# Performance work log

Measured on AMD Instinct MI355X. Metric: run time of the kernel, lower is better.

Reference implementation:

```python
import jax, jax.numpy as jnp
import numpy as np

T, B = 80, 256                 # timesteps (max objs per image), num sequences (images)
OBJ_DIM, EMBED, HID = 4096, 200, 512
NCLS = 151                      # 150 VG classes + background
D = HID + OBJ_DIM + EMBED + 128 # decoder inputs_dim = 4936


def _packed_gather_idx():
    # descending lengths 80..41, mimicking a sorted PackedSequence
    lengths = np.array([T - (i * 40) // B for i in range(B)])
    idx = []
    for t in range(T):
        bs = int((lengths > t).sum())
        idx.extend(t * B + b for b in range(bs))
    return np.asarray(idx, dtype=np.int32)  # [15504]


def setup_inputs() -> dict:
    key = jax.random.key(0)
    ks = jax.random.split(key, 6)
    s = jnp.float32(0.02)
    return {
        "sequence": jax.random.normal(ks[0], (T, B, D), jnp.float32),
        "embed": jax.random.normal(ks[1], (NCLS + 1, EMBED), jnp.float32) * s,
        "W_in": jax.random.normal(ks[2], (6 * HID, D + EMBED), jnp.float32) * s,
        "b_in": jnp.zeros((6 * HID,), jnp.float32),
        "W_state": jax.random.normal(ks[3], (5 * HID, HID), jnp.float32) * s,
        "b_state": jnp.zeros((5 * HID,), jnp.float32),
        "W_out": jax.random.normal(ks[4], (NCLS, HID), jnp.float32) * s,
        "b_out": jnp.zeros((NCLS,), jnp.float32),
        "gather_idx": jnp.asarray(_packed_gather_idx()),
    }


def reference(sequence, embed, W_in, b_in, W_state, b_state, W_out, b_out, gather_idx):
    H = HID

    def step(carry, x_t):
        h, c, prev_embed = carry
        ti = jnp.concatenate([x_t, prev_embed], axis=1)          # [B, D+E]
        pi = ti @ W_in.T + b_in                                   # [B, 6H]
        ps = h @ W_state.T + b_state                              # [B, 5H]
        i_g = jax.nn.sigmoid(pi[:, 0*H:1*H] + ps[:, 0*H:1*H])
        f_g = jax.nn.sigmoid(pi[:, 1*H:2*H] + ps[:, 1*H:2*H])
        m_i = jnp.tanh(pi[:, 2*H:3*H] + ps[:, 2*H:3*H])
        o_g = jax.nn.sigmoid(pi[:, 3*H:4*H] + ps[:, 3*H:4*H])
        c_new = i_g * m_i + f_g * c
        out = o_g * jnp.tanh(c_new)
        hw_g = jax.nn.sigmoid(pi[:, 4*H:5*H] + ps[:, 4*H:5*H])
        h_new = hw_g * out + (1.0 - hw_g) * pi[:, 5*H:6*H]        # highway
        pred = h_new @ W_out.T + b_out                            # [B, NCLS]
        # softmax is monotonic: argmax of softmax(pred)[:,1:] == argmax of pred[:,1:]
        best = jnp.argmax(pred[:, 1:], axis=1) + 1                # [B], in [1, NCLS-1]
        pe_new = embed[best + 1]                                  # [B, E]
        return (h_new, c_new, pe_new), (pred, best)

    h0 = jnp.zeros((B, HID), sequence.dtype)
    c0 = jnp.zeros((B, HID), sequence.dtype)
    pe0 = jnp.broadcast_to(embed[0], (B, EMBED))                  # 'start' token embed
    _, (dists, commits) = jax.lax.scan(step, (h0, c0, pe0), sequence)
    # packed (timestep-major) flattening of valid entries only
    out_dists = dists.reshape(T * B, NCLS)[gather_idx]            # [N, NCLS]
    out_commits = commits.reshape(T * B)[gather_idx]              # [N]
    return out_dists, out_commits
```

## Files before the change

### kernel.cpp

```cpp
#include <hip/hip_runtime.h>
#include <cstddef>
#include <cstdint>

#define T_STEPS 80
#define BATCH   256
#define DIM     4936
#define EMB     200
#define DE      5136
#define HID     512
#define SIXH    3072
#define FIVEH   2560
#define NCLS    151
#define NPACK   15504
#define NKT     156
#define NKT_H   16
#define NCOMB   2816
#define BUF2SZ  32768

typedef unsigned short ushort_t;
typedef short short8 __attribute__((ext_vector_type(8)));
typedef float f32x4 __attribute__((ext_vector_type(4)));
typedef float f32x16 __attribute__((ext_vector_type(16)));

__device__ inline ushort_t f2bf_rn(float x) {
    union { float f; uint32_t u; } v; v.f = x;
    uint32_t u = v.u;
    return (ushort_t)((u + 0x7FFFu + ((u >> 16) & 1u)) >> 16);
}
__device__ inline float bf2f(ushort_t b) {
    union { float f; uint32_t u; } v; v.u = ((uint32_t)b) << 16;
    return v.f;
}
__device__ inline float sigmoidf(float x) { return 1.f / (1.f + expf(-x)); }

__global__ __launch_bounds__(256) void convert_split(
    const float* __restrict__ src, int ld, int kvalid,
    ushort_t* __restrict__ hi, ushort_t* __restrict__ lo, int nktiles)
{
    __shared__ float s[128][33];
    const int tid = threadIdx.x;
    const int kt  = blockIdx.x;
    const int mt  = blockIdx.y;

#pragma unroll
    for (int it = 0; it < 4; ++it) {
        int idx = it * 256 + tid;
        int row = idx >> 3;
        int f4  = idx & 7;
        int k   = kt * 32 + f4 * 4;
        const float* p = src + (size_t)(mt * 128 + row) * ld + k;
        float4 v;
        if (k + 3 < kvalid) v = *(const float4*)p;
        else {
            v.x = (k + 0) < kvalid ? p[0] : 0.f;
            v.y = (k + 1) < kvalid ? p[1] : 0.f;
            v.z = (k + 2) < kvalid ? p[2] : 0.f;
            v.w = (k + 3) < kvalid ? p[3] : 0.f;
        }
        s[row][f4 * 4 + 0] = v.x; s[row][f4 * 4 + 1] = v.y;
        s[row][f4 * 4 + 2] = v.z; s[row][f4 * 4 + 3] = v.w;
    }
    __syncthreads();

    const size_t base = ((size_t)mt * nktiles + kt) * 4096;
#pragma unroll
    for (int it = 0; it < 2; ++it) {
        int o   = it * 256 + tid;
        int kb  = o >> 7;
        int row = o & 127;
        alignas(16) ushort_t hbuf[8];
        alignas(16) ushort_t lbuf[8];
#pragma unroll
        for (int e = 0; e < 8; ++e) {
            float x = s[row][kb * 8 + e];
            ushort_t hh = f2bf_rn(x);
            float lof = x - bf2f(hh);
            hbuf[e] = hh;
            lbuf[e] = f2bf_rn(lof);
        }
        *(uint4*)(hi + base + (size_t)o * 8) = *(const uint4*)hbuf;
        *(uint4*)(lo + base + (size_t)o * 8) = *(const uint4*)lbuf;
    }
}

__device__ inline void gload16(const ushort_t* g, ushort_t* l) {
    __builtin_amdgcn_global_load_lds(
        (const __attribute__((address_space(1))) void*)g,
        (__attribute__((address_space(3))) void*)l, 16, 0, 0);
}

__global__ __launch_bounds__(512, 1) void mfma3(
    const ushort_t* __restrict__ Ah, const ushort_t* __restrict__ Al,
    const ushort_t* __restrict__ Bh, const ushort_t* __restrict__ Bl,
    const float* __restrict__ bias, float* __restrict__ OUT,
    int nkt, int ldout, int nt)
{
    extern __shared__ __align__(16) ushort_t smem[];

    const int tid  = threadIdx.x;
    const int wave = tid >> 6;
    const int lane = tid & 63;

    int mtb, ntb;
    {
        const int L = blockIdx.x;
        if ((nt & 7) == 0) {
            const int x = L & 7;
            const int s = L >> 3;
            mtb = x + 8 * (s / 12);
            ntb = s % 12;
        } else {
            mtb = L / 12;
            ntb = L % 12;
        }
    }
    const int wr = wave >> 2;
    const int wc = wave & 3;

    f32x16 acc[4][2];
#pragma unroll
    for (int i = 0; i < 4; ++i)
#pragma unroll
        for (int j = 0; j < 2; ++j)
#pragma unroll
            for (int r = 0; r < 16; ++r) acc[i][j][r] = 0.f;

    const size_t a0 = (size_t)(2 * mtb) * nkt * 4096;
    const size_t a1 = a0 + (size_t)nkt * 4096;
    const size_t b0 = (size_t)(2 * ntb) * nkt * 4096;
    const size_t b1 = b0 + (size_t)nkt * 4096;

#define STAGE2(slot, kt_) do {                                      \
        ushort_t* d = smem + (slot) * BUF2SZ;                       \
        const size_t ko = (size_t)(kt_) * 4096 + tid * 8;           \
        gload16(Ah + a0 + ko, d + tid * 8);                         \
        gload16(Ah + a1 + ko, d + 4096 + tid * 8);                  \
        gload16(Al + a0 + ko, d + 8192 + tid * 8);                  \
        gload16(Al + a1 + ko, d + 12288 + tid * 8);                 \
        gload16(Bh + b0 + ko, d + 16384 + tid * 8);                 \
        gload16(Bh + b1 + ko, d + 20480 + tid * 8);                 \
        gload16(Bl + b0 + ko, d + 24576 + tid * 8);                 \
        gload16(Bl + b1 + ko, d + 28672 + tid * 8);                 \
    } while (0)

    const int lrow = lane & 31;
    const int kg   = lane >> 5;
    const int aBase = wr * 4096;
    const int bBase = 16384 + (wc >> 1) * 4096;
    const int bCol  = (wc & 1) * 64;

    STAGE2(0, 0);

    for (int kt = 0; kt < nkt; ++kt) {
        asm volatile("s_waitcnt vmcnt(0)" ::: "memory");
        __builtin_amdgcn_sched_barrier(0);
        __builtin_amdgcn_s_barrier();
        if (kt + 1 < nkt) STAGE2((kt + 1) & 1, kt + 1);

        const ushort_t* p = smem + (kt & 1) * BUF2SZ;
#pragma unroll
        for (int kh = 0; kh < 2; ++kh) {
            const int ko = (kh * 2 + kg) * 1024;
            short8 a_h[4], a_l[4], b_h[2], b_l[2];
#pragma unroll
            for (int ms = 0; ms < 4; ++ms) {
                const int ao = aBase + ko + (ms * 32 + lrow) * 8;
                a_h[ms] = *(const short8*)&p[ao];
                a_l[ms] = *(const short8*)&p[8192 + ao];
            }
#pragma unroll
            for (int ns = 0; ns < 2; ++ns) {
                const int bo = bBase + ko + (bCol + ns * 32 + lrow) * 8;
                b_h[ns] = *(const short8*)&p[bo];
                b_l[ns] = *(const short8*)&p[8192 + bo];
            }
#pragma unroll
            for (int ms = 0; ms < 4; ++ms)
#pragma unroll
                for (int ns = 0; ns < 2; ++ns) {
                    acc[ms][ns] = __builtin_amdgcn_mfma_f32_32x32x16_bf16(a_h[ms], b_h[ns], acc[ms][ns], 0, 0, 0);
                    acc[ms][ns] = __builtin_amdgcn_mfma_f32_32x32x16_bf16(a_h[ms], b_l[ns], acc[ms][ns], 0, 0, 0);
                    acc[ms][ns] = __builtin_amdgcn_mfma_f32_32x32x16_bf16(a_l[ms], b_h[ns], acc[ms][ns], 0, 0, 0);
                }
        }
    }
#undef STAGE2

#pragma unroll
    for (int ms = 0; ms < 4; ++ms)
#pragma unroll
        for (int ns = 0; ns < 2; ++ns) {
            const int col = ntb * 256 + wc * 64 + ns * 32 + (lane & 31);
            const float bv = bias[col];
            const int rowb = mtb * 256 + wr * 128 + ms * 32 + 4 * (lane >> 5);
#pragma unroll
            for (int r = 0; r < 16; ++r) {
                const int row = rowb + (r & 3) + 8 * (r >> 2);
                OUT[(size_t)row * ldout + col] = acc[ms][ns][r] + bv;
            }
        }
}

__global__ __launch_bounds__(256) void ps_full(
    const ushort_t* __restrict__ hH, const ushort_t* __restrict__ hL,
    const ushort_t* __restrict__ WcH, const ushort_t* __restrict__ WcL,
    const float* __restrict__ bias_comb,
    float* __restrict__ psF)
{
    __shared__ ushort_t sAh[8192], sAl[8192], sBh[8192], sBl[8192];

    const int tid  = threadIdx.x;
    const int wave = tid >> 6;
    const int lane = tid & 63;
    const int ntile = blockIdx.x;
    const int mtile = blockIdx.y;
    const int amt = mtile >> 1, arh = mtile & 1;
    const int bmt = ntile >> 1, brh = ntile & 1;
    const int wr = wave >> 1, wc = wave & 1;

    f32x4 acc[2][2];
#pragma unroll
    for (int i = 0; i < 2; ++i)
#pragma unroll
        for (int j = 0; j < 2; ++j) acc[i][j] = (f32x4){0.f, 0.f, 0.f, 0.f};

    const int lw    = wave * 512;
    const int lsrcA = wave * 1024 + arh * 512 + lane * 8;
    const int lsrcB = wave * 1024 + brh * 512 + lane * 8;
    const int kb = lane >> 4;
    const int lr = lane & 15;

    for (int r4nd = 0; r4nd < 4; ++r4nd) {
        if (r4nd) __syncthreads();
#pragma unroll
        for (int ki = 0; ki < 4; ++ki) {
            const int kt = r4nd * 4 + ki;
            const size_t atile = ((size_t)(amt * NKT_H + kt)) * 4096;
            const size_t btile = ((size_t)(bmt * NKT_H + kt)) * 4096;
            gload16(hH  + atile + lsrcA, &sAh[ki * 2048 + lw]);
            gload16(hL  + atile + lsrcA, &sAl[ki * 2048 + lw]);
            gload16(WcH + btile + lsrcB, &sBh[ki * 2048 + lw]);
            gload16(WcL + btile + lsrcB, &sBl[ki * 2048 + lw]);
        }
        __syncthreads();

#pragma unroll
        for (int ki = 0; ki < 4; ++ki) {
            short8 ah[2], al[2], bh[2], bl[2];
#pragma unroll
            for (int i = 0; i < 2; ++i) {
                const int ao = ki * 2048 + kb * 512 + (wr * 32 + i * 16 + lr) * 8;
                ah[i] = *(const short8*)&sAh[ao];
                al[i] = *(const short8*)&sAl[ao];
            }
#pragma unroll
            for (int j = 0; j < 2; ++j) {
                const int bo = ki * 2048 + kb * 512 + (wc * 32 + j * 16 + lr) * 8;
                bh[j] = *(const short8*)&sBh[bo];
                bl[j] = *(const short8*)&sBl[bo];
            }
#pragma unroll
            for (int i = 0; i < 2; ++i)
#pragma unroll
                for (int j = 0; j < 2; ++j) {
                    acc[i][j] = __builtin_amdgcn_mfma_f32_16x16x32_bf16(ah[i], bh[j], acc[i][j], 0, 0, 0);
                    acc[i][j] = __builtin_amdgcn_mfma_f32_16x16x32_bf16(ah[i], bl[j], acc[i][j], 0, 0, 0);
                    acc[i][j] = __builtin_amdgcn_mfma_f32_16x16x32_bf16(al[i], bh[j], acc[i][j], 0, 0, 0);
                }
        }
    }

    float* out = psF + (size_t)(mtile * 64) * NCOMB + ntile * 64;
#pragma unroll
    for (int i = 0; i < 2; ++i) {
        const int row = wr * 32 + i * 16 + (lane >> 4) * 4;
#pragma unroll
        for (int j = 0; j < 2; ++j) {
            const int col = wc * 32 + j * 16 + (lane & 15);
            const float bv = bias_comb[ntile * 64 + col];
#pragma unroll
            for (int r = 0; r < 4; ++r)
                out[(size_t)(row + r) * NCOMB + col] = acc[i][j][r] + bv;
        }
    }
}

__global__ __launch_bounds__(256) void ew_gemm(
    const float* __restrict__ embed, const float* __restrict__ Win,
    float* __restrict__ EW)
{
    __shared__ float As[16][68];
    __shared__ float Bs[16][68];
    const int tid = threadIdx.x;
    const int tx  = tid & 15;
    const int ty  = tid >> 4;
    const int n0  = blockIdx.x * 64;
    const int m0  = blockIdx.y * 64;
    const int lrow = tid >> 2;
    const int lk   = (tid & 3) * 4;

    float acc[4][4];
#pragma unroll
    for (int i = 0; i < 4; ++i)
#pragma unroll
        for (int j = 0; j < 4; ++j) acc[i][j] = 0.f;

    for (int k0 = 0; k0 < EMB; k0 += 16) {
        int k = k0 + lk;
        float4 av = {0.f,0.f,0.f,0.f}, bv = {0.f,0.f,0.f,0.f};
        if (k < EMB) {
            int am = m0 + lrow;
            if (am < 152) av = *(const float4*)(embed + (size_t)am * EMB + k);
            bv = *(const float4*)(Win + (size_t)(n0 + lrow) * DE + DIM + k);
        }
        __syncthreads();
        As[lk + 0][lrow] = av.x; As[lk + 1][lrow] = av.y;
        As[lk + 2][lrow] = av.z; As[lk + 3][lrow] = av.w;
        Bs[lk + 0][lrow] = bv.x; Bs[lk + 1][lrow] = bv.y;
        Bs[lk + 2][lrow] = bv.z; Bs[lk + 3][lrow] = bv.w;
        __syncthreads();
#pragma unroll
        for (int kk = 0; kk < 16; ++kk) {
            float4 a4 = *(const float4*)&As[kk][ty * 4];
            float4 b4 = *(const float4*)&Bs[kk][tx * 4];
            float avr[4] = {a4.x, a4.y, a4.z, a4.w};
            float bvr[4] = {b4.x, b4.y, b4.z, b4.w};
#pragma unroll
            for (int i = 0; i < 4; ++i)
#pragma unroll
                for (int j = 0; j < 4; ++j)
                    acc[i][j] = fmaf(avr[i], bvr[j], acc[i][j]);
        }
    }
#pragma unroll
    for (int i = 0; i < 4; ++i) {
        int m = m0 + ty * 4 + i;
        if (m < 152) {
#pragma unroll
            for (int j = 0; j < 4; ++j)
                EW[(size_t)m * SIXH + n0 + tx * 4 + j] = acc[i][j];
        }
    }
}

__global__ __launch_bounds__(256) void prep_misc(
    const float* __restrict__ Wout, const float* __restrict__ b_state,
    const float* __restrict__ b_out,
    float* __restrict__ padW, float* __restrict__ bc)
{
    int i = blockIdx.x * 256 + threadIdx.x;
    if (i < 256 * 512) {
        int row = i >> 9;
        padW[i] = (row < NCLS) ? Wout[i] : 0.f;
    }
    if (i < NCOMB) {
        float v;
        if (i < FIVEH)                 v = b_state[i];
        else if (i - FIVEH < NCLS)     v = b_out[i - FIVEH];
        else                           v = 0.f;
        bc[i] = v;
    }
}

__global__ __launch_bounds__(256) void init_state(
    float* __restrict__ c, ushort_t* __restrict__ hHt, ushort_t* __restrict__ hLt)
{
    int i = blockIdx.x * 256 + threadIdx.x;
    if (i < BATCH * HID) { c[i] = 0.f; hHt[i] = 0; hLt[i] = 0; }
}

__global__ __launch_bounds__(256) void step_fused(
    const float* __restrict__ px_t,
    const float* __restrict__ EW,
    const float* __restrict__ psF,
    int first,
    ushort_t* __restrict__ hHt, ushort_t* __restrict__ hLt,
    float* __restrict__ c, float* __restrict__ hF,
    float* __restrict__ dists_prev,
    int*   __restrict__ commit_prev)
{
    __shared__ float hs[HID];
    __shared__ float preds_s[NCLS + 1];
    __shared__ int   commit_sh;

    const int tid = threadIdx.x;
    const int b   = blockIdx.x;

    int erow = 0;
    if (!first) {
        if (tid < NCLS) {
            float pr = psF[(size_t)b * NCOMB + 2560 + tid];
            preds_s[tid] = pr;
            dists_prev[(size_t)b * NCLS + tid] = pr;
        }
        __syncthreads();
        if (tid < 64) {
            float bv = -__builtin_inff();
            int   bi = NCLS;
            for (int n = 1 + tid; n < NCLS; n += 64) {
                float v = preds_s[n];
                if (v > bv) { bv = v; bi = n; }
            }
#pragma unroll
            for (int off = 32; off; off >>= 1) {
                float ov = __shfl_down(bv, off);
                int   oi = __shfl_down(bi, off);
                if (ov > bv || (ov == bv && oi < bi)) { bv = ov; bi = oi; }
            }
            if (tid == 0) {
                commit_prev[b] = bi;
                commit_sh = bi;
            }
        }
        __syncthreads();
        erow = commit_sh + 1;
    }

    const float* ew = EW + (size_t)erow * SIXH;
    const float* px = px_t + (size_t)b * SIXH;
    const float* pp = psF + (size_t)b * NCOMB;

#pragma unroll
    for (int it = 0; it < 2; ++it) {
        const int u = it * 256 + tid;
        float p[6];
#pragma unroll
        for (int k2 = 0; k2 < 5; ++k2) {
            const int o = k2 * HID + u;
            p[k2] = px[o] + ew[o] + pp[o];
        }
        p[5] = px[5 * HID + u] + ew[5 * HID + u];

        float i_g = sigmoidf(p[0]);
        float f_g = sigmoidf(p[1]);
        float m_i = tanhf(p[2]);
        float o_g = sigmoidf(p[3]);
        float c_new = i_g * m_i + f_g * c[(size_t)b * HID + u];
        float outv  = o_g * tanhf(c_new);
        float hw    = sigmoidf(p[4]);
        float h_new = hw * outv + (1.f - hw) * p[5];
        c[(size_t)b * HID + u]  = c_new;
        hF[(size_t)b * HID + u] = h_new;
        hs[u] = h_new;
    }
    __syncthreads();

    if (tid < 128) {
        const int half = tid >> 6;
        const int ch   = tid & 63;
        const int mt   = b >> 7;
        const int row  = b & 127;
        const size_t off = ((size_t)(mt * NKT_H + (ch >> 2))) * 4096
                         + (size_t)(ch & 3) * 1024 + (size_t)row * 8;
        alignas(16) ushort_t buf[8];
        if (half == 0) {
#pragma unroll
            for (int e = 0; e < 8; ++e) buf[e] = f2bf_rn(hs[ch * 8 + e]);
            *(uint4*)(hHt + off) = *(const uint4*)buf;
        } else {
#pragma unroll
            for (int e = 0; e < 8; ++e) {
                float x = hs[ch * 8 + e];
                buf[e] = f2bf_rn(x - bf2f(f2bf_rn(x)));
            }
            *(uint4*)(hLt + off) = *(const uint4*)buf;
        }
    }
}

__global__ __launch_bounds__(192) void finalize_last(
    const float* __restrict__ hF, const float* __restrict__ Wout,
    const float* __restrict__ b_out,
    float* __restrict__ dists_last, int* __restrict__ commits_last)
{
    __shared__ float hsh[HID];
    __shared__ float preds[NCLS + 1];
    const int b = blockIdx.x;
    const int tid = threadIdx.x;

    if (tid < 128) {
        float4 v = *(const float4*)(hF + (size_t)b * HID + tid * 4);
        *(float4*)&hsh[tid * 4] = v;
    }
    __syncthreads();
    if (tid < NCLS) {
        const float* w = Wout + (size_t)tid * HID;
        float s0 = 0.f, s1 = 0.f, s2 = 0.f, s3 = 0.f;
        for (int k = 0; k < HID; k += 4) {
            float4 w4 = *(const float4*)(w + k);
            float4 h4 = *(const float4*)&hsh[k];
            s0 = fmaf(h4.x, w4.x, s0);
            s1 = fmaf(h4.y, w4.y, s1);
            s2 = fmaf(h4.z, w4.z, s2);
            s3 = fmaf(h4.w, w4.w, s3);
        }
        float s = b_out[tid] + ((s0 + s1) + (s2 + s3));
        preds[tid] = s;
        dists_last[(size_t)b * NCLS + tid] = s;
    }
    __syncthreads();
    if (tid == 0) {
        int bi = 1; float bv = preds[1];
        for (int n = 2; n < NCLS; ++n) {
            float v = preds[n];
            if (v > bv) { bv = v; bi = n; }
        }
        commits_last[b] = bi;
    }
}

__global__ __launch_bounds__(192) void gather_out(
    const float* __restrict__ dists, const int* __restrict__ commits,
    const int* __restrict__ gidx, float* __restrict__ out)
{
    const int i = blockIdx.x;
    const int g = gidx[i];
    if (threadIdx.x < NCLS)
        out[(size_t)i * NCLS + threadIdx.x] = dists[(size_t)g * NCLS + threadIdx.x];
    if (threadIdx.x == NCLS)
        out[(size_t)NPACK * NCLS + i] = (float)commits[g];
}

extern "C" void kernel_launch(void* const* d_in, const int* in_sizes, int n_in,
                              void* d_out, int out_size, void* d_ws, size_t ws_size,
                              hipStream_t stream)
{
    const float* X      = (const float*)d_in[0];
    const float* embed  = (const float*)d_in[1];
    const float* Win    = (const float*)d_in[2];
    const float* b_in   = (const float*)d_in[3];
    const float* Wst    = (const float*)d_in[4];
    const float* b_st   = (const float*)d_in[5];
    const float* Wout   = (const float*)d_in[6];
    const float* b_out  = (const float*)d_in[7];
    const int*   gidx   = (const int*)d_in[8];

    hipFuncSetAttribute((const void*)mfma3,
                        hipFuncAttributeMaxDynamicSharedMemorySize,
                        2 * BUF2SZ * 2);

    const size_t WN  = (size_t)24 * NKT * 4096;
    const size_t WCN = (size_t)22 * NKT_H * 4096;
    const size_t HN  = (size_t)2 * NKT_H * 4096;

    ushort_t* Wh  = (ushort_t*)d_ws;
    ushort_t* Wl  = Wh + WN;
    ushort_t* WcH = Wl + WN;
    ushort_t* WcL = WcH + WCN;
    ushort_t* hHt = WcL + WCN;
    ushort_t* hLt = hHt + HN;
    float* EW      = (float*)(hLt + HN);
    float* psF     = EW + (size_t)152 * SIXH;
    float* bc      = psF + (size_t)BATCH * NCOMB;
    float* c       = bc + NCOMB;
    float* hF      = c + (size_t)BATCH * HID;
    float* padW    = hF + (size_t)BATCH * HID;
    float* dists   = padW + (size_t)256 * HID;
    int* commits   = (int*)(dists + (size_t)T_STEPS * BATCH * NCLS);
    char* cbase    = (char*)(commits + T_STEPS * BATCH);

    size_t off = (size_t)(cbase - (char*)d_ws);
    off = (off + 255) & ~(size_t)255;
    const size_t per_t = (size_t)2 * 2 * NKT * 4096 * 2 + (size_t)BATCH * SIXH * 4;
    size_t rem = (ws_size > off) ? (ws_size - off) : 0;
    int CT = (int)(rem / per_t);
    if (CT > T_STEPS) CT = T_STEPS;
    if (CT < 1) CT = 1;

    ushort_t* Xh = (ushort_t*)((char*)d_ws + off);
    ushort_t* Xl = Xh + (size_t)2 * CT * NKT * 4096;
    float* px    = (float*)(Xl + (size_t)2 * CT * NKT * 4096);

    convert_split<<<dim3(NKT, 24), 256, 0, stream>>>(Win, DE, DIM, Wh, Wl, NKT);
    convert_split<<<dim3(NKT_H, 20), 256, 0, stream>>>(Wst, HID, HID, WcH, WcL, NKT_H);
    prep_misc<<<512, 256, 0, stream>>>(Wout, b_st, b_out, padW, bc);
    convert_split<<<dim3(NKT_H, 2), 256, 0, stream>>>(
        padW, HID, HID, WcH + (size_t)20 * NKT_H * 4096, WcL + (size_t)20 * NKT_H * 4096, NKT_H);
    ew_gemm<<<dim3(SIXH / 64, 3), 256, 0, stream>>>(embed, Win, EW);
    init_state<<<512, 256, 0, stream>>>(c, hHt, hLt);

    for (int t0 = 0; t0 < T_STEPS; t0 += CT) {
        int nt = T_STEPS - t0;
        if (nt > CT) nt = CT;
        convert_split<<<dim3(NKT, 2 * nt), 256, 0, stream>>>(
            X + (size_t)t0 * BATCH * DIM, DIM, DIM, Xh, Xl, NKT);
        mfma3<<<dim3((SIXH / 256) * nt), 512, 2 * BUF2SZ * 2, stream>>>(
            Xh, Xl, Wh, Wl, b_in, px, NKT, SIXH, nt);
        for (int t = t0; t < t0 + nt; ++t) {
            const int tp = (t > 0) ? t - 1 : 0;
            ps_full<<<dim3(44, 4), 256, 0, stream>>>(
                hHt, hLt, WcH, WcL, bc, psF);
            step_fused<<<BATCH, 256, 0, stream>>>(
                px + (size_t)(t - t0) * BATCH * SIXH, EW, psF,
                (t == 0) ? 1 : 0, hHt, hLt, c, hF,
                dists + (size_t)tp * BATCH * NCLS, commits + (size_t)tp * BATCH);
        }
    }

    finalize_last<<<BATCH, 192, 0, stream>>>(
        hF, Wout, b_out,
        dists + (size_t)(T_STEPS - 1) * BATCH * NCLS,
        commits + (size_t)(T_STEPS - 1) * BATCH);

    gather_out<<<NPACK, 192, 0, stream>>>(dists, commits, gidx, (float*)d_out);
}
```

Measured before the change: 2.994 ms.

## Single-buffer LDS in mfma3 to fit two blocks per CU

Replaces the double-buffered 128KB dynamic LDS staging in the big input-projection GEMM with a single 64KB static buffer, and raises launch bounds to two blocks per CU. Each k-tile is now loaded, waited on, computed, and fenced with a barrier, so there is no prefetch overlap inside a block. The intent is to hide load latency through two co-resident blocks instead. This risks register pressure under the tighter launch bound, since the 4x2 f32x16 accumulators alone take 128 VGPRs, and it adds a stall on every tile when occupancy does not actually reach two.

```diff
diff --git a/kernel.cpp b/kernel.cpp
--- a/kernel.cpp
+++ b/kernel.cpp
@@ -89,13 +89,13 @@
         (__attribute__((address_space(3))) void*)l, 16, 0, 0);
 }
 
-__global__ __launch_bounds__(512, 1) void mfma3(
+__global__ __launch_bounds__(512, 2) void mfma3(
     const ushort_t* __restrict__ Ah, const ushort_t* __restrict__ Al,
     const ushort_t* __restrict__ Bh, const ushort_t* __restrict__ Bl,
     const float* __restrict__ bias, float* __restrict__ OUT,
     int nkt, int ldout, int nt)
 {
-    extern __shared__ __align__(16) ushort_t smem[];
+    __shared__ __align__(16) ushort_t smem[BUF2SZ];
 
     const int tid  = threadIdx.x;
     const int wave = tid >> 6;
@@ -130,17 +130,16 @@
     const size_t b0 = (size_t)(2 * ntb) * nkt * 4096;
     const size_t b1 = b0 + (size_t)nkt * 4096;
 
-#define STAGE2(slot, kt_) do {                                      \
-        ushort_t* d = smem + (slot) * BUF2SZ;                       \
+#define STAGE1(kt_) do {                                            \
         const size_t ko = (size_t)(kt_) * 4096 + tid * 8;           \
-        gload16(Ah + a0 + ko, d + tid * 8);                         \
-        gload16(Ah + a1 + ko, d + 4096 + tid * 8);                  \
-        gload16(Al + a0 + ko, d + 8192 + tid * 8);                  \
-        gload16(Al + a1 + ko, d + 12288 + tid * 8);                 \
-        gload16(Bh + b0 + ko, d + 16384 + tid * 8);                 \
-        gload16(Bh + b1 + ko, d + 20480 + tid * 8);                 \
-        gload16(Bl + b0 + ko, d + 24576 + tid * 8);                 \
-        gload16(Bl + b1 + ko, d + 28672 + tid * 8);                 \
+        gload16(Ah + a0 + ko, smem + tid * 8);                      \
+        gload16(Ah + a1 + ko, smem + 4096 + tid * 8);               \
+        gload16(Al + a0 + ko, smem + 8192 + tid * 8);               \
+        gload16(Al + a1 + ko, smem + 12288 + tid * 8);              \
+        gload16(Bh + b0 + ko, smem + 16384 + tid * 8);              \
+        gload16(Bh + b1 + ko, smem + 20480 + tid * 8);              \
+        gload16(Bl + b0 + ko, smem + 24576 + tid * 8);              \
+        gload16(Bl + b1 + ko, smem + 28672 + tid * 8);              \
     } while (0)
 
     const int lrow = lane & 31;
@@ -149,15 +148,12 @@
     const int bBase = 16384 + (wc >> 1) * 4096;
     const int bCol  = (wc & 1) * 64;
 
-    STAGE2(0, 0);
-
     for (int kt = 0; kt < nkt; ++kt) {
+        STAGE1(kt);
         asm volatile("s_waitcnt vmcnt(0)" ::: "memory");
         __builtin_amdgcn_sched_barrier(0);
         __builtin_amdgcn_s_barrier();
-        if (kt + 1 < nkt) STAGE2((kt + 1) & 1, kt + 1);
-
-        const ushort_t* p = smem + (kt & 1) * BUF2SZ;
+
 #pragma unroll
         for (int kh = 0; kh < 2; ++kh) {
             const int ko = (kh * 2 + kg) * 1024;
@@ -165,14 +161,14 @@
 #pragma unroll
             for (int ms = 0; ms < 4; ++ms) {
                 const int ao = aBase + ko + (ms * 32 + lrow) * 8;
-                a_h[ms] = *(const short8*)&p[ao];
-                a_l[ms] = *(const short8*)&p[8192 + ao];
+                a_h[ms] = *(const short8*)&smem[ao];
+                a_l[ms] = *(const short8*)&smem[8192 + ao];
             }
 #pragma unroll
             for (int ns = 0; ns < 2; ++ns) {
                 const int bo = bBase + ko + (bCol + ns * 32 + lrow) * 8;
-                b_h[ns] = *(const short8*)&p[bo];
-                b_l[ns] = *(const short8*)&p[8192 + bo];
+                b_h[ns] = *(const short8*)&smem[bo];
+                b_l[ns] = *(const short8*)&smem[8192 + bo];
             }
 #pragma unroll
             for (int ms = 0; ms < 4; ++ms)
@@ -183,8 +179,9 @@
                     acc[ms][ns] = __builtin_amdgcn_mfma_f32_32x32x16_bf16(a_l[ms], b_h[ns], acc[ms][ns], 0, 0, 0);
                 }
         }
-    }
-#undef STAGE2
+        __builtin_amdgcn_s_barrier();
+    }
+#undef STAGE1
 
 #pragma unroll
     for (int ms = 0; ms < 4; ++ms)
@@ -534,10 +531,6 @@
     const float* Wout   = (const float*)d_in[6];
     const float* b_out  = (const float*)d_in[7];
     const int*   gidx   = (const int*)d_in[8];
-
-    hipFuncSetAttribute((const void*)mfma3,
-                        hipFuncAttributeMaxDynamicSharedMemorySize,
-                        2 * BUF2SZ * 2);
 
     const size_t WN  = (size_t)24 * NKT * 4096;
     const size_t WCN = (size_t)22 * NKT_H * 4096;
@@ -584,7 +577,7 @@
         if (nt > CT) nt = CT;
         convert_split<<<dim3(NKT, 2 * nt), 256, 0, stream>>>(
             X + (size_t)t0 * BATCH * DIM, DIM, DIM, Xh, Xl, NKT);
-        mfma3<<<dim3((SIXH / 256) * nt), 512, 2 * BUF2SZ * 2, stream>>>(
+        mfma3<<<dim3((SIXH / 256) * nt), 512, 0, stream>>>(
             Xh, Xl, Wh, Wl, b_in, px, NKT, SIXH, nt);
         for (int t = t0; t < t0 + nt; ++t) {
             const int tp = (t > 0) ? t - 1 : 0;
```

Result: slower. 3.261 ms (+8.9%).

## Double-buffer ps_full LDS staging and hoist step_fused loads before argmax

Applied to the files above, without the earlier changes.

The recurrent-state GEMM kernel now stages its K chunks into two dynamic-LDS buffers, so the global-to-LDS loads for the next chunk are issued while the current chunk is being multiplied, with a single barrier per round instead of two. The step kernel issues its loads of px, psF and c into registers before the argmax reduction, so their latency is hidden behind the reduction and its barriers. This doubles LDS use to 128 KB and adds launch_bounds occupancy of 1, which could limit occupancy. Correctness now depends on the manual vmcnt wait and barrier ordering.

```diff
diff --git a/kernel.cpp b/kernel.cpp
--- a/kernel.cpp
+++ b/kernel.cpp
@@ -16,6 +16,7 @@
 #define NKT_H   16
 #define NCOMB   2816
 #define BUF2SZ  32768
+#define PSBUF   32768
 
 typedef unsigned short ushort_t;
 typedef short short8 __attribute__((ext_vector_type(8)));
@@ -201,13 +202,13 @@
         }
 }
 
-__global__ __launch_bounds__(256) void ps_full(
+__global__ __launch_bounds__(256, 1) void ps_full(
     const ushort_t* __restrict__ hH, const ushort_t* __restrict__ hL,
     const ushort_t* __restrict__ WcH, const ushort_t* __restrict__ WcL,
     const float* __restrict__ bias_comb,
     float* __restrict__ psF)
 {
-    __shared__ ushort_t sAh[8192], sAl[8192], sBh[8192], sBl[8192];
+    extern __shared__ __align__(16) ushort_t psmem[];
 
     const int tid  = threadIdx.x;
     const int wave = tid >> 6;
@@ -230,34 +231,43 @@
     const int kb = lane >> 4;
     const int lr = lane & 15;
 
-    for (int r4nd = 0; r4nd < 4; ++r4nd) {
-        if (r4nd) __syncthreads();
-#pragma unroll
-        for (int ki = 0; ki < 4; ++ki) {
-            const int kt = r4nd * 4 + ki;
-            const size_t atile = ((size_t)(amt * NKT_H + kt)) * 4096;
-            const size_t btile = ((size_t)(bmt * NKT_H + kt)) * 4096;
-            gload16(hH  + atile + lsrcA, &sAh[ki * 2048 + lw]);
-            gload16(hL  + atile + lsrcA, &sAl[ki * 2048 + lw]);
-            gload16(WcH + btile + lsrcB, &sBh[ki * 2048 + lw]);
-            gload16(WcL + btile + lsrcB, &sBl[ki * 2048 + lw]);
-        }
-        __syncthreads();
-
+#define STAGE_PS(slot, r_) do {                                           \
+        ushort_t* d = psmem + (slot) * PSBUF;                             \
+        _Pragma("unroll")                                                 \
+        for (int ki_ = 0; ki_ < 4; ++ki_) {                               \
+            const int kt_ = (r_) * 4 + ki_;                               \
+            const size_t at_ = ((size_t)(amt * NKT_H + kt_)) * 4096;      \
+            const size_t bt_ = ((size_t)(bmt * NKT_H + kt_)) * 4096;      \
+            gload16(hH  + at_ + lsrcA, d + ki_ * 2048 + lw);              \
+            gload16(hL  + at_ + lsrcA, d + 8192 + ki_ * 2048 + lw);       \
+            gload16(WcH + bt_ + lsrcB, d + 16384 + ki_ * 2048 + lw);      \
+            gload16(WcL + bt_ + lsrcB, d + 24576 + ki_ * 2048 + lw);      \
+        }                                                                 \
+    } while (0)
+
+    STAGE_PS(0, 0);
+
+    for (int r = 0; r < 4; ++r) {
+        asm volatile("s_waitcnt vmcnt(0)" ::: "memory");
+        __builtin_amdgcn_sched_barrier(0);
+        __builtin_amdgcn_s_barrier();
+        if (r + 1 < 4) STAGE_PS((r + 1) & 1, r + 1);
+
+        const ushort_t* p = psmem + (r & 1) * PSBUF;
 #pragma unroll
         for (int ki = 0; ki < 4; ++ki) {
             short8 ah[2], al[2], bh[2], bl[2];
 #pragma unroll
             for (int i = 0; i < 2; ++i) {
                 const int ao = ki * 2048 + kb * 512 + (wr * 32 + i * 16 + lr) * 8;
-                ah[i] = *(const short8*)&sAh[ao];
-                al[i] = *(const short8*)&sAl[ao];
+                ah[i] = *(const short8*)&p[ao];
+                al[i] = *(const short8*)&p[8192 + ao];
             }
 #pragma unroll
             for (int j = 0; j < 2; ++j) {
                 const int bo = ki * 2048 + kb * 512 + (wc * 32 + j * 16 + lr) * 8;
-                bh[j] = *(const short8*)&sBh[bo];
-                bl[j] = *(const short8*)&sBl[bo];
+                bh[j] = *(const short8*)&p[16384 + bo];
+                bl[j] = *(const short8*)&p[24576 + bo];
             }
 #pragma unroll
             for (int i = 0; i < 2; ++i)
@@ -269,6 +279,7 @@
                 }
         }
     }
+#undef STAGE_PS
 
     float* out = psF + (size_t)(mtile * 64) * NCOMB + ntile * 64;
 #pragma unroll
@@ -386,10 +397,26 @@
     const int tid = threadIdx.x;
     const int b   = blockIdx.x;
 
+    const float* px = px_t + (size_t)b * SIXH;
+    const float* pp = psF + (size_t)b * NCOMB;
+
+    float pxv[2][6], ppv[2][5], cv[2];
+#pragma unroll
+    for (int it = 0; it < 2; ++it) {
+        const int u = it * 256 + tid;
+#pragma unroll
+        for (int k2 = 0; k2 < 5; ++k2) {
+            pxv[it][k2] = px[k2 * HID + u];
+            ppv[it][k2] = pp[k2 * HID + u];
+        }
+        pxv[it][5] = px[5 * HID + u];
+        cv[it] = c[(size_t)b * HID + u];
+    }
+
     int erow = 0;
     if (!first) {
         if (tid < NCLS) {
-            float pr = psF[(size_t)b * NCOMB + 2560 + tid];
+            float pr = pp[2560 + tid];
             preds_s[tid] = pr;
             dists_prev[(size_t)b * NCLS + tid] = pr;
         }
@@ -417,25 +444,21 @@
     }
 
     const float* ew = EW + (size_t)erow * SIXH;
-    const float* px = px_t + (size_t)b * SIXH;
-    const float* pp = psF + (size_t)b * NCOMB;
 
 #pragma unroll
     for (int it = 0; it < 2; ++it) {
         const int u = it * 256 + tid;
         float p[6];
 #pragma unroll
-        for (int k2 = 0; k2 < 5; ++k2) {
-            const int o = k2 * HID + u;
-            p[k2] = px[o] + ew[o] + pp[o];
-        }
-        p[5] = px[5 * HID + u] + ew[5 * HID + u];
+        for (int k2 = 0; k2 < 5; ++k2)
+            p[k2] = pxv[it][k2] + ew[k2 * HID + u] + ppv[it][k2];
+        p[5] = pxv[it][5] + ew[5 * HID + u];
 
         float i_g = sigmoidf(p[0]);
         float f_g = sigmoidf(p[1]);
         float m_i = tanhf(p[2]);
         float o_g = sigmoidf(p[3]);
-        float c_new = i_g * m_i + f_g * c[(size_t)b * HID + u];
+        float c_new = i_g * m_i + f_g * cv[it];
         float outv  = o_g * tanhf(c_new);
         float hw    = sigmoidf(p[4]);
         float h_new = hw * outv + (1.f - hw) * p[5];
@@ -538,6 +561,9 @@
     hipFuncSetAttribute((const void*)mfma3,
                         hipFuncAttributeMaxDynamicSharedMemorySize,
                         2 * BUF2SZ * 2);
+    hipFuncSetAttribute((const void*)ps_full,
+                        hipFuncAttributeMaxDynamicSharedMemorySize,
+                        2 * PSBUF * 2);
 
     const size_t WN  = (size_t)24 * NKT * 4096;
     const size_t WCN = (size_t)22 * NKT_H * 4096;
@@ -588,7 +614,7 @@
             Xh, Xl, Wh, Wl, b_in, px, NKT, SIXH, nt);
         for (int t = t0; t < t0 + nt; ++t) {
             const int tp = (t > 0) ? t - 1 : 0;
-            ps_full<<<dim3(44, 4), 256, 0, stream>>>(
+            ps_full<<<dim3(44, 4), 256, 2 * PSBUF * 2, stream>>>(
                 hHt, hLt, WcH, WcL, bc, psF);
             step_fused<<<BATCH, 256, 0, stream>>>(
                 px + (size_t)(t - t0) * BATCH * SIXH, EW, psF,
```

Measured after the change: 2.901 ms, median of 2. -3.1%, faster.
